# Kernel optimization log

Hardware: AMD Instinct MI355X
Metric: run time of the kernel (lower is better)

Reference implementation:

```python
import jax, jax.numpy as jnp
import numpy as np

DIM = 256
N_HEADS = 4
B, N = 2, 4096


def setup_inputs() -> dict:
    key = jax.random.key(0)
    ks = jax.random.split(key, 10)
    s = DIM ** -0.5
    return {
        "x": jax.random.normal(ks[0], (B, N, DIM), dtype=jnp.float32),
        "q_w": jax.random.normal(ks[1], (DIM, DIM), dtype=jnp.float32) * s,
        "q_b": jnp.zeros((DIM,), dtype=jnp.float32),
        "k_w": jax.random.normal(ks[2], (DIM, DIM), dtype=jnp.float32) * s,
        "k_b": jnp.zeros((DIM,), dtype=jnp.float32),
        "v_w": jax.random.normal(ks[3], (DIM, DIM), dtype=jnp.float32) * s,
        "v_b": jnp.zeros((DIM,), dtype=jnp.float32),
        "o_w": jax.random.normal(ks[4], (DIM, DIM), dtype=jnp.float32) * s,
        "o_b": jnp.zeros((DIM,), dtype=jnp.float32),
        "tau": jnp.ones((1,), dtype=jnp.float32),
    }


def reference(x, q_w, q_b, k_w, k_b, v_w, v_b, o_w, o_b, tau):
    Bsz, Nlen, C = x.shape
    H = N_HEADS
    Dh = C // H
    scale = C ** -0.5  # source uses full dim, not head_dim
    Q = (x @ q_w.T + q_b).reshape(Bsz, Nlen, H, Dh)
    K = (x @ k_w.T + k_b).reshape(Bsz, Nlen, H, Dh)
    V = (x @ v_w.T + v_b).reshape(Bsz, Nlen, H, Dh)
    attn = jnp.einsum('bnhd,bmhd->bhnm', Q, K) * scale
    # soft-threshold gate: keep only |attn| > tau, then relu
    attn = jax.nn.relu(jnp.where(jnp.abs(attn) > tau, attn, 0.0))
    attn = jax.nn.softmax(attn, axis=-1)
    out = jnp.einsum('bhnm,bmhd->bnhd', attn, V).reshape(Bsz, Nlen, C)
    return out @ o_w.T + o_b
```

## Files before the change

kernel.cpp:

```cpp
#include <hip/hip_runtime.h>

#define SEQ   4096
#define CDIM  256
#define NHEAD 4
#define DHEAD 64
#define PSTRIDE 72
#define LOG2E 1.4426950408889634f

typedef float    f32x4 __attribute__((ext_vector_type(4)));
typedef _Float16 f16x8 __attribute__((ext_vector_type(8)));
typedef _Float16 f16x4 __attribute__((ext_vector_type(4)));
typedef _Float16 f16x2 __attribute__((ext_vector_type(2)));

__device__ __forceinline__ f16x8 cvt_frag(const float* __restrict__ p) {
    float4 f0 = *(const float4*)p;
    float4 f1 = *(const float4*)(p + 4);
    f16x8 r;
    r[0]=(_Float16)f0.x; r[1]=(_Float16)f0.y; r[2]=(_Float16)f0.z; r[3]=(_Float16)f0.w;
    r[4]=(_Float16)f1.x; r[5]=(_Float16)f1.y; r[6]=(_Float16)f1.z; r[7]=(_Float16)f1.w;
    return r;
}

__device__ __forceinline__ f16x2 pkrtz(float a, float b) {
    return __builtin_bit_cast(f16x2, __builtin_amdgcn_cvt_pkrtz(a, b));
}

__global__ __launch_bounds__(256) void sta_prep(
    const float* __restrict__ qw, const float* __restrict__ kw,
    const float* __restrict__ vw, const float* __restrict__ ow,
    _Float16* __restrict__ w16)
{
    const int mat = blockIdx.y;
    const float* src = (mat == 0) ? qw : (mat == 1) ? kw : (mat == 2) ? vw : ow;
    const int i = (blockIdx.x * 256 + threadIdx.x) * 8;
    *(f16x8*)(w16 + mat * 65536 + i) = cvt_frag(src + i);
}

__global__ __launch_bounds__(256) void sta_qkv(
    const float* __restrict__ x, const _Float16* __restrict__ w16,
    const float* __restrict__ qb, const float* __restrict__ kb, const float* __restrict__ vb,
    _Float16* __restrict__ Qo, _Float16* __restrict__ Ko, _Float16* __restrict__ Vo)
{
    const int wave = threadIdx.x >> 6;
    const int lane = threadIdx.x & 63;
    const int l15  = lane & 15;
    const int quad = lane >> 4;
    const int mat  = blockIdx.y;
    const int half = blockIdx.z;
    const int row0 = blockIdx.x * 64 + wave * 16;

    const _Float16* w    = w16 + mat * 65536;
    const float*    bias = (mat == 0) ? qb : (mat == 1) ? kb : vb;

    f16x8 xf[8];
    const float* xrow = x + (row0 + l15) * CDIM + quad * 8;
    #pragma unroll
    for (int ks = 0; ks < 8; ks++) xf[ks] = cvt_frag(xrow + ks * 32);

    #pragma unroll 1
    for (int ct = 0; ct < 8; ct++) {
        const int ctg = half * 8 + ct;
        const _Float16* wr = w + (ctg * 16 + l15) * CDIM + quad * 8;
        f32x4 acc = {0.f, 0.f, 0.f, 0.f};
        if (mat < 2) {
            #pragma unroll
            for (int ks = 0; ks < 8; ks++)
                acc = __builtin_amdgcn_mfma_f32_16x16x32_f16(*(const f16x8*)(wr + ks * 32), xf[ks], acc, 0, 0, 0);
            const float4 bv = *(const float4*)(bias + ctg * 16 + quad * 4);
            const int c0 = ctg * 16 + quad * 4;
            const int h = c0 >> 6, d0 = c0 & 63;
            const int grow = row0 + l15, b = grow >> 12, n = grow & (SEQ - 1);
            const float sc = (mat == 0) ? (0.0625f * LOG2E) : 1.0f;
            f16x4 o;
            o[0] = (_Float16)((acc[0] + bv.x) * sc);
            o[1] = (_Float16)((acc[1] + bv.y) * sc);
            o[2] = (_Float16)((acc[2] + bv.z) * sc);
            o[3] = (_Float16)((acc[3] + bv.w) * sc);
            _Float16* dst = ((mat == 0) ? Qo : Ko) + (((b * NHEAD + h) * SEQ + n) * DHEAD + d0);
            *(f16x4*)dst = o;
        } else {
            #pragma unroll
            for (int ks = 0; ks < 8; ks++)
                acc = __builtin_amdgcn_mfma_f32_16x16x32_f16(xf[ks], *(const f16x8*)(wr + ks * 32), acc, 0, 0, 0);
            const int c = ctg * 16 + l15;
            const int h = c >> 6, d = c & 63;
            const float bv = bias[c];
            const int grow0 = row0 + quad * 4, b = grow0 >> 12, n0 = grow0 & (SEQ - 1);
            f16x4 o;
            #pragma unroll
            for (int r = 0; r < 4; r++) o[r] = (_Float16)(acc[r] + bv);
            *(f16x4*)(Vo + (((b * NHEAD + h) * DHEAD + d) * SEQ + n0)) = o;
        }
    }
}

__global__ __launch_bounds__(64) void sta_attn(
    const _Float16* __restrict__ Q, const _Float16* __restrict__ K, const _Float16* __restrict__ Vt,
    const float* __restrict__ taup,
    float* __restrict__ Opart, float* __restrict__ lpart)
{
    __shared__ __align__(16) _Float16 pbuf[2 * 64 * PSTRIDE];

    const int lane = threadIdx.x;
    const int l15  = lane & 15;
    const int quad = lane >> 4;
    const int qt = blockIdx.x;
    const int bh = blockIdx.y;
    const int sp = blockIdx.z;
    const float tau2 = __builtin_bit_cast(float, __builtin_amdgcn_readfirstlane(
        __builtin_bit_cast(int, fmaxf(taup[0], 0.0f) * LOG2E)));

    const _Float16* Qb = Q  + bh * SEQ * DHEAD;
    const _Float16* Kb = K  + bh * SEQ * DHEAD;
    const _Float16* Vb = Vt + bh * DHEAD * SEQ;

    const int q0 = qt * 64;

    _Float16* pw_base = pbuf + l15 * PSTRIDE + quad * 4;
    const _Float16* pr_base = pbuf + l15 * PSTRIDE + quad * 8;
    const _Float16* Krow = Kb + l15 * DHEAD + quad * 8;
    const _Float16* Vrow = Vb + l15 * SEQ + quad * 8;

    f16x8 qf[4][2];
    #pragma unroll
    for (int qb = 0; qb < 4; qb++)
        #pragma unroll
        for (int ks = 0; ks < 2; ks++)
            qf[qb][ks] = *(const f16x8*)(Qb + (q0 + qb * 16 + l15) * DHEAD + ks * 32 + quad * 8);

    f32x4 O[4][4];
    #pragma unroll
    for (int qb = 0; qb < 4; qb++)
        #pragma unroll
        for (int db = 0; db < 4; db++) O[qb][db] = (f32x4){0.f, 0.f, 0.f, 0.f};
    float rs[4] = {0.f, 0.f, 0.f, 0.f};

    const int kt0 = sp * 16;

    {
        const _Float16* Kt = Krow + (kt0 * 64) * DHEAD;
        #pragma unroll
        for (int kb = 0; kb < 4; kb++) {
            f16x8 k0 = *(const f16x8*)(Kt + kb * 16 * DHEAD);
            f16x8 k1 = *(const f16x8*)(Kt + kb * 16 * DHEAD + 32);
            #pragma unroll
            for (int qb = 0; qb < 4; qb++) {
                f32x4 a = {0.f, 0.f, 0.f, 0.f};
                a = __builtin_amdgcn_mfma_f32_16x16x32_f16(k0, qf[qb][0], a, 0, 0, 0);
                a = __builtin_amdgcn_mfma_f32_16x16x32_f16(k1, qf[qb][1], a, 0, 0, 0);
                float p0 = (a[0] > tau2) ? __builtin_amdgcn_exp2f(a[0]) : 1.0f;
                float p1 = (a[1] > tau2) ? __builtin_amdgcn_exp2f(a[1]) : 1.0f;
                float p2 = (a[2] > tau2) ? __builtin_amdgcn_exp2f(a[2]) : 1.0f;
                float p3 = (a[3] > tau2) ? __builtin_amdgcn_exp2f(a[3]) : 1.0f;
                rs[qb] += (p0 + p1) + (p2 + p3);
                f16x2 lo = pkrtz(p0, p1);
                f16x2 hi = pkrtz(p2, p3);
                f16x4 pk;
                pk[0] = lo[0]; pk[1] = lo[1]; pk[2] = hi[0]; pk[3] = hi[1];
                *(f16x4*)(pw_base + qb * 16 * PSTRIDE + kb * 16) = pk;
            }
        }
    }

    #pragma unroll 1
    for (int t = 1; t < 16; t++) {
        const int kvc = (kt0 + t) * 64;
        const int kvp = kvc - 64;
        _Float16* pw = pw_base + (t & 1) * (64 * PSTRIDE);
        const _Float16* pr = pr_base + ((t & 1) ^ 1) * (64 * PSTRIDE);
        const _Float16* Kt = Krow + kvc * DHEAD;
        f16x8 pa[4];
        #pragma unroll
        for (int c = 0; c < 4; c++) {
            f16x8 k0 = *(const f16x8*)(Kt + c * 16 * DHEAD);
            f16x8 k1 = *(const f16x8*)(Kt + c * 16 * DHEAD + 32);
            #pragma unroll
            for (int qb = 0; qb < 4; qb++) {
                f32x4 a = {0.f, 0.f, 0.f, 0.f};
                a = __builtin_amdgcn_mfma_f32_16x16x32_f16(k0, qf[qb][0], a, 0, 0, 0);
                a = __builtin_amdgcn_mfma_f32_16x16x32_f16(k1, qf[qb][1], a, 0, 0, 0);
                float p0 = (a[0] > tau2) ? __builtin_amdgcn_exp2f(a[0]) : 1.0f;
                float p1 = (a[1] > tau2) ? __builtin_amdgcn_exp2f(a[1]) : 1.0f;
                float p2 = (a[2] > tau2) ? __builtin_amdgcn_exp2f(a[2]) : 1.0f;
                float p3 = (a[3] > tau2) ? __builtin_amdgcn_exp2f(a[3]) : 1.0f;
                rs[qb] += (p0 + p1) + (p2 + p3);
                f16x2 lo = pkrtz(p0, p1);
                f16x2 hi = pkrtz(p2, p3);
                f16x4 pk;
                pk[0] = lo[0]; pk[1] = lo[1]; pk[2] = hi[0]; pk[3] = hi[1];
                *(f16x4*)(pw + qb * 16 * PSTRIDE + c * 16) = pk;
            }
            const int ks = c >> 1, db0 = (c & 1) * 2;
            if ((c & 1) == 0) {
                #pragma unroll
                for (int qb = 0; qb < 4; qb++)
                    pa[qb] = *(const f16x8*)(pr + qb * 16 * PSTRIDE + ks * 32);
            }
            #pragma unroll
            for (int dd = 0; dd < 2; dd++) {
                const int db = db0 + dd;
                f16x8 vf = *(const f16x8*)(Vrow + db * 16 * SEQ + kvp + ks * 32);
                #pragma unroll
                for (int qb = 0; qb < 4; qb++)
                    O[qb][db] = __builtin_amdgcn_mfma_f32_16x16x32_f16(pa[qb], vf, O[qb][db], 0, 0, 0);
            }
        }
    }

    {
        const int kvp = (kt0 + 15) * 64;
        const _Float16* pr = pr_base + (15 & 1) * (64 * PSTRIDE);
        #pragma unroll
        for (int ks = 0; ks < 2; ks++) {
            f16x8 pa[4];
            #pragma unroll
            for (int qb = 0; qb < 4; qb++)
                pa[qb] = *(const f16x8*)(pr + qb * 16 * PSTRIDE + ks * 32);
            #pragma unroll
            for (int db = 0; db < 4; db++) {
                f16x8 vf = *(const f16x8*)(Vrow + db * 16 * SEQ + kvp + ks * 32);
                #pragma unroll
                for (int qb = 0; qb < 4; qb++)
                    O[qb][db] = __builtin_amdgcn_mfma_f32_16x16x32_f16(pa[qb], vf, O[qb][db], 0, 0, 0);
            }
        }
    }

    #pragma unroll
    for (int qb = 0; qb < 4; qb++) {
        float v = rs[qb];
        v += __shfl_xor(v, 16);
        v += __shfl_xor(v, 32);
        rs[qb] = v;
    }
    float* Ob = Opart + (size_t)((sp * 8 + bh) * SEQ + q0) * DHEAD;
    #pragma unroll
    for (int qb = 0; qb < 4; qb++)
        #pragma unroll
        for (int db = 0; db < 4; db++)
            #pragma unroll
            for (int r = 0; r < 4; r++)
                Ob[(qb * 16 + quad * 4 + r) * DHEAD + db * 16 + l15] = O[qb][db][r];
    if (quad == 0) {
        #pragma unroll
        for (int qb = 0; qb < 4; qb++)
            lpart[(sp * 8 + bh) * SEQ + q0 + qb * 16 + l15] = rs[qb];
    }
}

__global__ __launch_bounds__(128) void sta_oproj2(
    const float* __restrict__ Opart, const float* __restrict__ lpart,
    const _Float16* __restrict__ w16o, const float* __restrict__ ob,
    float* __restrict__ out)
{
    const int wave = threadIdx.x >> 6;
    const int lane = threadIdx.x & 63;
    const int l15  = lane & 15;
    const int quad = lane >> 4;
    const int row0 = blockIdx.x * 32 + wave * 16;

    const int nglob = row0 + l15;
    const int b = nglob >> 12, n = nglob & (SEQ - 1);

    f16x8 af[8];
    #pragma unroll
    for (int h = 0; h < 4; h++) {
        const int bhh = b * NHEAD + h;
        float lsum = 0.f;
        #pragma unroll
        for (int s = 0; s < 4; s++) lsum += lpart[(s * 8 + bhh) * SEQ + n];
        const float inv = 1.0f / lsum;
        #pragma unroll
        for (int dp = 0; dp < 2; dp++) {
            const int dh0 = dp * 32 + quad * 8;
            float a0x=0.f,a0y=0.f,a0z=0.f,a0w=0.f,a1x=0.f,a1y=0.f,a1z=0.f,a1w=0.f;
            #pragma unroll
            for (int s = 0; s < 4; s++) {
                const float* p = Opart + (size_t)((s * 8 + bhh) * SEQ + n) * DHEAD + dh0;
                const float4 t0 = *(const float4*)p;
                const float4 t1 = *(const float4*)(p + 4);
                a0x += t0.x; a0y += t0.y; a0z += t0.z; a0w += t0.w;
                a1x += t1.x; a1y += t1.y; a1z += t1.z; a1w += t1.w;
            }
            f16x8 v;
            v[0] = (_Float16)(a0x * inv); v[1] = (_Float16)(a0y * inv);
            v[2] = (_Float16)(a0z * inv); v[3] = (_Float16)(a0w * inv);
            v[4] = (_Float16)(a1x * inv); v[5] = (_Float16)(a1y * inv);
            v[6] = (_Float16)(a1z * inv); v[7] = (_Float16)(a1w * inv);
            af[h * 2 + dp] = v;
        }
    }

    #pragma unroll 1
    for (int ct = 0; ct < 16; ct++) {
        const _Float16* wr = w16o + (ct * 16 + l15) * CDIM + quad * 8;
        f32x4 acc = {0.f, 0.f, 0.f, 0.f};
        #pragma unroll
        for (int ks = 0; ks < 8; ks++)
            acc = __builtin_amdgcn_mfma_f32_16x16x32_f16(*(const f16x8*)(wr + ks * 32), af[ks], acc, 0, 0, 0);
        const int c0 = ct * 16 + quad * 4;
        const float4 bv = *(const float4*)(ob + c0);
        float4 res;
        res.x = acc[0] + bv.x; res.y = acc[1] + bv.y;
        res.z = acc[2] + bv.z; res.w = acc[3] + bv.w;
        *(float4*)(out + (size_t)nglob * CDIM + c0) = res;
    }
}

extern "C" void kernel_launch(void* const* d_in, const int* in_sizes, int n_in,
                              void* d_out, int out_size, void* d_ws, size_t ws_size,
                              hipStream_t stream) {
    const float* x   = (const float*)d_in[0];
    const float* qw  = (const float*)d_in[1];
    const float* qb  = (const float*)d_in[2];
    const float* kw  = (const float*)d_in[3];
    const float* kb  = (const float*)d_in[4];
    const float* vw  = (const float*)d_in[5];
    const float* vb  = (const float*)d_in[6];
    const float* ow  = (const float*)d_in[7];
    const float* ob  = (const float*)d_in[8];
    const float* tau = (const float*)d_in[9];

    _Float16* w16 = (_Float16*)d_ws;
    _Float16* Q   = w16 + 262144;
    _Float16* K   = Q + 2097152;
    _Float16* Vt  = K + 2097152;
    float* Opart  = (float*)(Vt + 2097152);
    float* lpart  = Opart + 8388608;

    sta_prep  <<<dim3(32, 4),      256, 0, stream>>>(qw, kw, vw, ow, w16);
    sta_qkv   <<<dim3(128, 3, 2),  256, 0, stream>>>(x, w16, qb, kb, vb, Q, K, Vt);
    sta_attn  <<<dim3(64, 8, 4),    64, 0, stream>>>(Q, K, Vt, tau, Opart, lpart);
    sta_oproj2<<<256,              128, 0, stream>>>(Opart, lpart, w16 + 3 * 65536, ob, (float*)d_out);
}
```

Measured before the change: 195.9 us.

## Warp-specialize attention: one wave computes scores, another does PV and row sums

The attention block grows from one wave to two. Wave 0 computes QK^T, the threshold and exp, and writes P to double-buffered shared memory. Wave 1 runs the PV MFMAs for the previous tile and gets row sums from an MFMA against a ones vector. The two waves sync with __syncthreads every tile, which is meant to overlap exp/VALU work with the PV matrix work. In exchange it adds a barrier per tile, and the row sums are now taken from fp16-rounded P instead of fp32.

```diff
diff --git a/kernel.cpp b/kernel.cpp
--- a/kernel.cpp
+++ b/kernel.cpp
@@ -94,14 +94,15 @@
     }
 }
 
-__global__ __launch_bounds__(64) void sta_attn(
+__global__ __launch_bounds__(128) void sta_attn(
     const _Float16* __restrict__ Q, const _Float16* __restrict__ K, const _Float16* __restrict__ Vt,
     const float* __restrict__ taup,
     float* __restrict__ Opart, float* __restrict__ lpart)
 {
     __shared__ __align__(16) _Float16 pbuf[2 * 64 * PSTRIDE];
 
-    const int lane = threadIdx.x;
+    const int wv   = threadIdx.x >> 6;
+    const int lane = threadIdx.x & 63;
     const int l15  = lane & 15;
     const int quad = lane >> 4;
     const int qt = blockIdx.x;
@@ -115,6 +116,7 @@
     const _Float16* Vb = Vt + bh * DHEAD * SEQ;
 
     const int q0 = qt * 64;
+    const int kt0 = sp * 16;
 
     _Float16* pw_base = pbuf + l15 * PSTRIDE + quad * 4;
     const _Float16* pr_base = pbuf + l15 * PSTRIDE + quad * 8;
@@ -122,129 +124,111 @@
     const _Float16* Vrow = Vb + l15 * SEQ + quad * 8;
 
     f16x8 qf[4][2];
+    if (wv == 0) {
+        #pragma unroll
+        for (int qb = 0; qb < 4; qb++)
+            #pragma unroll
+            for (int ks = 0; ks < 2; ks++)
+                qf[qb][ks] = *(const f16x8*)(Qb + (q0 + qb * 16 + l15) * DHEAD + ks * 32 + quad * 8);
+    }
+
+    f32x4 O[4][4];
+    f32x4 accd[4];
     #pragma unroll
-    for (int qb = 0; qb < 4; qb++)
-        #pragma unroll
-        for (int ks = 0; ks < 2; ks++)
-            qf[qb][ks] = *(const f16x8*)(Qb + (q0 + qb * 16 + l15) * DHEAD + ks * 32 + quad * 8);
-
-    f32x4 O[4][4];
+    for (int qb = 0; qb < 4; qb++) {
+        accd[qb] = (f32x4){0.f, 0.f, 0.f, 0.f};
+        #pragma unroll
+        for (int db = 0; db < 4; db++) O[qb][db] = (f32x4){0.f, 0.f, 0.f, 0.f};
+    }
+    f16x8 ones;
     #pragma unroll
-    for (int qb = 0; qb < 4; qb++)
-        #pragma unroll
-        for (int db = 0; db < 4; db++) O[qb][db] = (f32x4){0.f, 0.f, 0.f, 0.f};
-    float rs[4] = {0.f, 0.f, 0.f, 0.f};
-
-    const int kt0 = sp * 16;
-
-    {
-        const _Float16* Kt = Krow + (kt0 * 64) * DHEAD;
-        #pragma unroll
-        for (int kb = 0; kb < 4; kb++) {
-            f16x8 k0 = *(const f16x8*)(Kt + kb * 16 * DHEAD);
-            f16x8 k1 = *(const f16x8*)(Kt + kb * 16 * DHEAD + 32);
-            #pragma unroll
-            for (int qb = 0; qb < 4; qb++) {
-                f32x4 a = {0.f, 0.f, 0.f, 0.f};
-                a = __builtin_amdgcn_mfma_f32_16x16x32_f16(k0, qf[qb][0], a, 0, 0, 0);
-                a = __builtin_amdgcn_mfma_f32_16x16x32_f16(k1, qf[qb][1], a, 0, 0, 0);
-                float p0 = (a[0] > tau2) ? __builtin_amdgcn_exp2f(a[0]) : 1.0f;
-                float p1 = (a[1] > tau2) ? __builtin_amdgcn_exp2f(a[1]) : 1.0f;
-                float p2 = (a[2] > tau2) ? __builtin_amdgcn_exp2f(a[2]) : 1.0f;
-                float p3 = (a[3] > tau2) ? __builtin_amdgcn_exp2f(a[3]) : 1.0f;
-                rs[qb] += (p0 + p1) + (p2 + p3);
-                f16x2 lo = pkrtz(p0, p1);
-                f16x2 hi = pkrtz(p2, p3);
-                f16x4 pk;
-                pk[0] = lo[0]; pk[1] = lo[1]; pk[2] = hi[0]; pk[3] = hi[1];
-                *(f16x4*)(pw_base + qb * 16 * PSTRIDE + kb * 16) = pk;
+    for (int j = 0; j < 8; j++) ones[j] = (_Float16)1.0f;
+
+    #pragma unroll 1
+    for (int t = 0; t < 16; t++) {
+        if (wv == 0) {
+            const _Float16* Kt = Krow + ((kt0 + t) * 64) * DHEAD;
+            _Float16* pw = pw_base + (t & 1) * (64 * PSTRIDE);
+            #pragma unroll
+            for (int kb = 0; kb < 4; kb++) {
+                f16x8 k0 = *(const f16x8*)(Kt + kb * 16 * DHEAD);
+                f16x8 k1 = *(const f16x8*)(Kt + kb * 16 * DHEAD + 32);
+                #pragma unroll
+                for (int qb = 0; qb < 4; qb++) {
+                    f32x4 a = {0.f, 0.f, 0.f, 0.f};
+                    a = __builtin_amdgcn_mfma_f32_16x16x32_f16(k0, qf[qb][0], a, 0, 0, 0);
+                    a = __builtin_amdgcn_mfma_f32_16x16x32_f16(k1, qf[qb][1], a, 0, 0, 0);
+                    float p0 = (a[0] > tau2) ? __builtin_amdgcn_exp2f(a[0]) : 1.0f;
+                    float p1 = (a[1] > tau2) ? __builtin_amdgcn_exp2f(a[1]) : 1.0f;
+                    float p2 = (a[2] > tau2) ? __builtin_amdgcn_exp2f(a[2]) : 1.0f;
+                    float p3 = (a[3] > tau2) ? __builtin_amdgcn_exp2f(a[3]) : 1.0f;
+                    f16x2 lo = pkrtz(p0, p1);
+                    f16x2 hi = pkrtz(p2, p3);
+                    f16x4 pk;
+                    pk[0] = lo[0]; pk[1] = lo[1]; pk[2] = hi[0]; pk[3] = hi[1];
+                    *(f16x4*)(pw + qb * 16 * PSTRIDE + kb * 16) = pk;
+                }
             }
-        }
-    }
-
-    #pragma unroll 1
-    for (int t = 1; t < 16; t++) {
-        const int kvc = (kt0 + t) * 64;
-        const int kvp = kvc - 64;
-        _Float16* pw = pw_base + (t & 1) * (64 * PSTRIDE);
-        const _Float16* pr = pr_base + ((t & 1) ^ 1) * (64 * PSTRIDE);
-        const _Float16* Kt = Krow + kvc * DHEAD;
-        f16x8 pa[4];
-        #pragma unroll
-        for (int c = 0; c < 4; c++) {
-            f16x8 k0 = *(const f16x8*)(Kt + c * 16 * DHEAD);
-            f16x8 k1 = *(const f16x8*)(Kt + c * 16 * DHEAD + 32);
-            #pragma unroll
-            for (int qb = 0; qb < 4; qb++) {
-                f32x4 a = {0.f, 0.f, 0.f, 0.f};
-                a = __builtin_amdgcn_mfma_f32_16x16x32_f16(k0, qf[qb][0], a, 0, 0, 0);
-                a = __builtin_amdgcn_mfma_f32_16x16x32_f16(k1, qf[qb][1], a, 0, 0, 0);
-                float p0 = (a[0] > tau2) ? __builtin_amdgcn_exp2f(a[0]) : 1.0f;
-                float p1 = (a[1] > tau2) ? __builtin_amdgcn_exp2f(a[1]) : 1.0f;
-                float p2 = (a[2] > tau2) ? __builtin_amdgcn_exp2f(a[2]) : 1.0f;
-                float p3 = (a[3] > tau2) ? __builtin_amdgcn_exp2f(a[3]) : 1.0f;
-                rs[qb] += (p0 + p1) + (p2 + p3);
-                f16x2 lo = pkrtz(p0, p1);
-                f16x2 hi = pkrtz(p2, p3);
-                f16x4 pk;
-                pk[0] = lo[0]; pk[1] = lo[1]; pk[2] = hi[0]; pk[3] = hi[1];
-                *(f16x4*)(pw + qb * 16 * PSTRIDE + c * 16) = pk;
-            }
-            const int ks = c >> 1, db0 = (c & 1) * 2;
-            if ((c & 1) == 0) {
+        } else if (t >= 1) {
+            const int kvp = (kt0 + t - 1) * 64;
+            const _Float16* pr = pr_base + ((t - 1) & 1) * (64 * PSTRIDE);
+            #pragma unroll
+            for (int ks = 0; ks < 2; ks++) {
+                f16x8 pa[4];
                 #pragma unroll
                 for (int qb = 0; qb < 4; qb++)
                     pa[qb] = *(const f16x8*)(pr + qb * 16 * PSTRIDE + ks * 32);
+                #pragma unroll
+                for (int db = 0; db < 4; db++) {
+                    f16x8 vf = *(const f16x8*)(Vrow + db * 16 * SEQ + kvp + ks * 32);
+                    #pragma unroll
+                    for (int qb = 0; qb < 4; qb++)
+                        O[qb][db] = __builtin_amdgcn_mfma_f32_16x16x32_f16(pa[qb], vf, O[qb][db], 0, 0, 0);
+                }
+                #pragma unroll
+                for (int qb = 0; qb < 4; qb++)
+                    accd[qb] = __builtin_amdgcn_mfma_f32_16x16x32_f16(pa[qb], ones, accd[qb], 0, 0, 0);
             }
-            #pragma unroll
-            for (int dd = 0; dd < 2; dd++) {
-                const int db = db0 + dd;
+        }
+        __syncthreads();
+    }
+
+    if (wv == 1) {
+        const int kvp = (kt0 + 15) * 64;
+        const _Float16* pr = pr_base + (15 & 1) * (64 * PSTRIDE);
+        #pragma unroll
+        for (int ks = 0; ks < 2; ks++) {
+            f16x8 pa[4];
+            #pragma unroll
+            for (int qb = 0; qb < 4; qb++)
+                pa[qb] = *(const f16x8*)(pr + qb * 16 * PSTRIDE + ks * 32);
+            #pragma unroll
+            for (int db = 0; db < 4; db++) {
                 f16x8 vf = *(const f16x8*)(Vrow + db * 16 * SEQ + kvp + ks * 32);
                 #pragma unroll
                 for (int qb = 0; qb < 4; qb++)
                     O[qb][db] = __builtin_amdgcn_mfma_f32_16x16x32_f16(pa[qb], vf, O[qb][db], 0, 0, 0);
             }
-        }
-    }
-
-    {
-        const int kvp = (kt0 + 15) * 64;
-        const _Float16* pr = pr_base + (15 & 1) * (64 * PSTRIDE);
-        #pragma unroll
-        for (int ks = 0; ks < 2; ks++) {
-            f16x8 pa[4];
             #pragma unroll
             for (int qb = 0; qb < 4; qb++)
-                pa[qb] = *(const f16x8*)(pr + qb * 16 * PSTRIDE + ks * 32);
-            #pragma unroll
-            for (int db = 0; db < 4; db++) {
-                f16x8 vf = *(const f16x8*)(Vrow + db * 16 * SEQ + kvp + ks * 32);
-                #pragma unroll
-                for (int qb = 0; qb < 4; qb++)
-                    O[qb][db] = __builtin_amdgcn_mfma_f32_16x16x32_f16(pa[qb], vf, O[qb][db], 0, 0, 0);
-            }
-        }
-    }
-
-    #pragma unroll
-    for (int qb = 0; qb < 4; qb++) {
-        float v = rs[qb];
-        v += __shfl_xor(v, 16);
-        v += __shfl_xor(v, 32);
-        rs[qb] = v;
-    }
-    float* Ob = Opart + (size_t)((sp * 8 + bh) * SEQ + q0) * DHEAD;
-    #pragma unroll
-    for (int qb = 0; qb < 4; qb++)
-        #pragma unroll
-        for (int db = 0; db < 4; db++)
-            #pragma unroll
-            for (int r = 0; r < 4; r++)
-                Ob[(qb * 16 + quad * 4 + r) * DHEAD + db * 16 + l15] = O[qb][db][r];
-    if (quad == 0) {
+                accd[qb] = __builtin_amdgcn_mfma_f32_16x16x32_f16(pa[qb], ones, accd[qb], 0, 0, 0);
+        }
+
+        float* Ob = Opart + (size_t)((sp * 8 + bh) * SEQ + q0) * DHEAD;
         #pragma unroll
         for (int qb = 0; qb < 4; qb++)
-            lpart[(sp * 8 + bh) * SEQ + q0 + qb * 16 + l15] = rs[qb];
+            #pragma unroll
+            for (int db = 0; db < 4; db++)
+                #pragma unroll
+                for (int r = 0; r < 4; r++)
+                    Ob[(qb * 16 + quad * 4 + r) * DHEAD + db * 16 + l15] = O[qb][db][r];
+        if (l15 == 0) {
+            #pragma unroll
+            for (int qb = 0; qb < 4; qb++)
+                #pragma unroll
+                for (int r = 0; r < 4; r++)
+                    lpart[(sp * 8 + bh) * SEQ + q0 + qb * 16 + quad * 4 + r] = accd[qb][r];
+        }
     }
 }
 
@@ -330,6 +314,6 @@
 
     sta_prep  <<<dim3(32, 4),      256, 0, stream>>>(qw, kw, vw, ow, w16);
     sta_qkv   <<<dim3(128, 3, 2),  256, 0, stream>>>(x, w16, qb, kb, vb, Q, K, Vt);
-    sta_attn  <<<dim3(64, 8, 4),    64, 0, stream>>>(Q, K, Vt, tau, Opart, lpart);
+    sta_attn  <<<dim3(64, 8, 4),   128, 0, stream>>>(Q, K, Vt, tau, Opart, lpart);
     sta_oproj2<<<256,              128, 0, stream>>>(Opart, lpart, w16 + 3 * 65536, ob, (float*)d_out);
 }
```

Result: slower. 202.0 us (+3.1%).
